# Optimization experiments

Measured on AMD Instinct MI355X. Metric: run time of the kernel, lower is better.

The kernel has to match this reference:

```python
import jax, jax.numpy as jnp
import numpy as np

L, B, T, H = 3, 128, 256, 512  # layers, batch, seq_max_len, n_hidden


def setup_inputs() -> dict:
    key = jax.random.key(0)
    k0, k1, k2 = jax.random.split(key, 3)
    scale = 1.0 / np.sqrt(H).astype(np.float32)
    x = jax.random.normal(k0, (B, T, H), jnp.float32)
    kernels = jax.random.normal(k1, (L, H, 3 * H), jnp.float32) * scale
    rec_kernels = jax.random.normal(k2, (L, H, 3 * H), jnp.float32) * scale
    biases = jnp.zeros((L, 2, 3 * H), jnp.float32)  # [input_bias, recurrent_bias] (reset_after=True)
    return {"x": x, "kernels": kernels, "rec_kernels": rec_kernels, "biases": biases}


def _gru_layer(x, h0, Wk, Wu, b):
    # x: [B,T,D], h0: [B,H], Wk: [D,3H], Wu: [H,3H], b: [2,3H]
    # Keras GRU, reset_after=True, gate order (z, r, h)
    xp = jnp.einsum('btd,dh->bth', x, Wk) + b[0]  # precompute input projections
    br = b[1]

    def step(h, xp_t):
        rec = h @ Wu + br                      # [B,3H]
        xz, xr, xh = jnp.split(xp_t, 3, axis=-1)
        rz, rr, rh = jnp.split(rec, 3, axis=-1)
        z = jax.nn.sigmoid(xz + rz)
        r = jax.nn.sigmoid(xr + rr)
        hh = jnp.tanh(xh + r * rh)
        h_new = z * h + (1.0 - z) * hh
        return h_new, h_new

    last_h, seq = jax.lax.scan(step, h0, jnp.swapaxes(xp, 0, 1))  # seq: [T,B,H]
    return jnp.swapaxes(seq, 0, 1), last_h


def reference(x, kernels, rec_kernels, biases):
    Bc, Tc, _ = x.shape
    Hd = kernels.shape[2] // 3
    state = None
    for l in range(kernels.shape[0]):
        # layer l>0 receives previous layer's final state as initial_state
        h0 = jnp.zeros((Bc, Hd), x.dtype) if state is None else state
        x, state = _gru_layer(x, h0, kernels[l], rec_kernels[l], biases[l])
    # tf.reshape(states, (-1, H)) then tf.split(seq_max_len, axis=0) -> stack == reshape to [T, B, H]
    states_h = x.reshape(-1, Hd).reshape(Tc, -1, Hd)
    return states_h, state
```

## Files before the change

### kernel.cpp

```cpp
#include <hip/hip_runtime.h>
#include <hip/hip_bf16.h>

#define NL  3
#define NB  128
#define NT  256
#define NH  512
#define NH3 1536
#define NBH (NB*NH)
#define NM  (NB*NT)

typedef __bf16 bf16x8 __attribute__((ext_vector_type(8)));
typedef float  floatx4 __attribute__((ext_vector_type(4)));
typedef __hip_bfloat16 bf16;
typedef unsigned long long u64;

__device__ __forceinline__ floatx4 mfma16(bf16x8 a, bf16x8 b, floatx4 c) {
  return __builtin_amdgcn_mfma_f32_16x16x32_bf16(a, b, c, 0, 0, 0);
}
__device__ __forceinline__ void gload16(const void* g, void* l) {
  __builtin_amdgcn_global_load_lds(
      (const __attribute__((address_space(1))) unsigned int*)g,
      (__attribute__((address_space(3))) unsigned int*)l, 16, 0, 0);
}
__device__ __forceinline__ float fsig(float x)  { return 1.0f / (1.0f + __expf(-x)); }
__device__ __forceinline__ float ftanh(float x) { return 2.0f / (1.0f + __expf(-2.0f*x)) - 1.0f; }
__device__ __forceinline__ float b2f(unsigned short u) {
  unsigned v = (unsigned)u << 16; float f; __builtin_memcpy(&f, &v, 4); return f;
}
__device__ __forceinline__ unsigned short f2b(float f) {
  bf16 h = __float2bfloat16(f); unsigned short u; __builtin_memcpy(&u, &h, 2); return u;
}
__device__ __forceinline__ u64 ald(const u64* p) {
  return __hip_atomic_load(p, __ATOMIC_RELAXED, __HIP_MEMORY_SCOPE_AGENT);
}
__device__ __forceinline__ void ast(u64* p, u64 v) {
  __hip_atomic_store(p, v, __ATOMIC_RELAXED, __HIP_MEMORY_SCOPE_AGENT);
}

__global__ void transpose_cvt_kernel(const float* __restrict__ in, bf16* __restrict__ out) {
  __shared__ float tile[32][33];
  int l = blockIdx.z;
  int n0 = blockIdx.x * 32, k0 = blockIdx.y * 32;
  const float* src = in + (size_t)l * NH * NH3;
  bf16* dst = out + (size_t)l * NH3 * NH;
  int tx = threadIdx.x, ty = threadIdx.y;
#pragma unroll
  for (int i = 0; i < 4; i++)
    tile[ty + 8*i][tx] = src[(size_t)(k0 + ty + 8*i) * NH3 + n0 + tx];
  __syncthreads();
#pragma unroll
  for (int i = 0; i < 4; i++)
    dst[(size_t)(n0 + ty + 8*i) * NH + k0 + tx] = __float2bfloat16(tile[tx][ty + 8*i]);
}

__global__ void cvt_x_kernel(const float* __restrict__ in, bf16* __restrict__ out) {
  size_t i = (size_t)blockIdx.x * blockDim.x + threadIdx.x;
  float4 v = ((const float4*)in)[i];
  ushort4 pk;
  pk.x = f2b(v.x); pk.y = f2b(v.y); pk.z = f2b(v.z); pk.w = f2b(v.w);
  ((ushort4*)out)[i] = pk;
}

__global__ void __launch_bounds__(256, 2) gemm_xp_kernel(
    const bf16* __restrict__ A, const bf16* __restrict__ Bt,
    const float* __restrict__ bias, bf16* __restrict__ C, int a_mode)
{
  __shared__ char alds[16384];
  __shared__ char blds[16384];
  int tid = threadIdx.x;
  int lane = tid & 63, w = tid >> 6;
  int mblk = blockIdx.x, nblk = blockIdx.y;
  int wm = w >> 1, wn = w & 1;
  int klane = (lane >> 4) * 8;
  int r0 = 2*w*16 + (lane & 15);
  size_t arow0, arow1;
  if (a_mode == 0) {
    arow0 = ((size_t)r0 * NT + mblk) * NH;
    arow1 = ((size_t)(r0 + 16) * NT + mblk) * NH;
  } else {
    arow0 = (size_t)(mblk*128 + r0) * NH;
    arow1 = arow0 + (size_t)16 * NH;
  }
  size_t brow0 = (size_t)(nblk*128 + 2*w*16 + (lane & 15)) * NH;
  size_t brow1 = brow0 + (size_t)16 * NH;

  floatx4 acc[4][4];
#pragma unroll
  for (int i = 0; i < 4; i++)
#pragma unroll
    for (int j = 0; j < 4; j++) acc[i][j] = (floatx4){0.f, 0.f, 0.f, 0.f};

  for (int kk = 0; kk < 8; kk++) {
    int kb = kk*64 + klane;
#pragma unroll
    for (int kt = 0; kt < 2; kt++) {
      int kg = kb + kt*32;
      gload16(A  + arow0 + kg, alds + (kt*8 + 2*w    ) * 1024);
      gload16(A  + arow1 + kg, alds + (kt*8 + 2*w + 1) * 1024);
      gload16(Bt + brow0 + kg, blds + (kt*8 + 2*w    ) * 1024);
      gload16(Bt + brow1 + kg, blds + (kt*8 + 2*w + 1) * 1024);
    }
    __syncthreads();
#pragma unroll
    for (int kt = 0; kt < 2; kt++) {
      bf16x8 af[4], bfr[4];
#pragma unroll
      for (int i = 0; i < 4; i++) af[i]  = *(const bf16x8*)(alds + ((kt*8 + wm*4 + i)*64 + lane)*16);
#pragma unroll
      for (int j = 0; j < 4; j++) bfr[j] = *(const bf16x8*)(blds + ((kt*8 + wn*4 + j)*64 + lane)*16);
#pragma unroll
      for (int i = 0; i < 4; i++)
#pragma unroll
        for (int j = 0; j < 4; j++)
          acc[i][j] = mfma16(af[i], bfr[j], acc[i][j]);
    }
    __syncthreads();
  }
  int cl = lane & 15, rbase = (lane >> 4) * 4;
#pragma unroll
  for (int i = 0; i < 4; i++) {
    int gm = mblk*128 + wm*64 + i*16 + rbase;
#pragma unroll
    for (int j = 0; j < 4; j++) {
      int gn = nblk*128 + wn*64 + j*16 + cl;
      float bv = bias[gn];
#pragma unroll
      for (int r = 0; r < 4; r++)
        C[(size_t)(gm + r) * NH3 + gn] = __float2bfloat16(acc[i][j][r] + bv);
    }
  }
}

__global__ void __launch_bounds__(512, 2) gru_scan_kernel(
    const bf16*  __restrict__ wuT,
    const float* __restrict__ br,
    const bf16*  __restrict__ xp,
    bf16*        __restrict__ seq,
    float*       __restrict__ hlast,
    float*       __restrict__ out,
    unsigned*    __restrict__ cnt,
    unsigned tgtbase, int layer)
{
  __shared__ __align__(16) char h_raw[16384];
  __shared__ int deadflag;
  int tid = threadIdx.x, lane = tid & 63, w = tid >> 6;
  int g = blockIdx.x >> 2, c = blockIdx.x & 3;
  int bb0 = g * 16;
  int r16 = lane & 15, h4 = lane >> 4;
  int srow = tid & 15, ssc = tid >> 4;
  if (tid == 0) deadflag = 0;

  bf16x8 wf[3][16];
  float  bv[3][4];
#pragma unroll
  for (int G = 0; G < 3; G++) {
    const bf16* wrow = wuT + ((size_t)(G*NH + c*128 + w*16 + r16)) * NH + h4*8;
#pragma unroll
    for (int kt = 0; kt < 16; kt++) wf[G][kt] = *(const bf16x8*)(wrow + kt*32);
#pragma unroll
    for (int q = 0; q < 4; q++) bv[G][q] = br[G*NH + c*128 + w*16 + h4*4 + q];
  }

  float hreg[4];
  if (layer == 0) {
    hreg[0] = hreg[1] = hreg[2] = hreg[3] = 0.0f;
  } else {
    const float* hsrc = hlast + (size_t)(bb0 + r16) * NH + c*128 + w*16 + h4*4;
    float4 v = *(const float4*)hsrc;
    hreg[0] = v.x; hreg[1] = v.y; hreg[2] = v.z; hreg[3] = v.w;
  }

  u64* seqU = (u64*)seq;

  for (int t = 0; t < NT; t++) {
    const u64* xq = (const u64*)(xp + ((size_t)t*NB + bb0 + r16)*NH3 + c*128 + w*16 + h4*4);
    u64 xv0 = xq[0], xv1 = xq[128], xv2 = xq[256];

    if (t > 0) {
      if (tid == 0) {
        unsigned tgt = tgtbase + 4u * (unsigned)t;
        long sp = 0;
        while (__hip_atomic_load(cnt + g, __ATOMIC_RELAXED, __HIP_MEMORY_SCOPE_AGENT) < tgt) {
          __builtin_amdgcn_s_sleep(1);
          if (++sp > (1L << 22)) { deadflag = 1; break; }
        }
      }
      __syncthreads();
      if (deadflag) return;
    }

    if (layer == 0 && t == 0) {
      *(int4*)(h_raw + tid*32)      = (int4){0,0,0,0};
      *(int4*)(h_raw + tid*32 + 16) = (int4){0,0,0,0};
    } else {
      int slot = (t == 0) ? NT : t;
      const u64* src = seqU + ((size_t)slot*NBH + (size_t)(bb0 + srow)*NH) / 4;
#pragma unroll
      for (int d = 0; d < 2; d++) {
        int sc = ssc + d*32;
        u64 q0 = ald(src + sc*2), q1 = ald(src + sc*2 + 1);
        u64* dst = (u64*)(h_raw + (((sc >> 2)*64) + (sc & 3)*16 + srow)*16);
        dst[0] = q0; dst[1] = q1;
      }
    }
    __syncthreads();

    floatx4 ac0 = (floatx4){0,0,0,0}, ac1 = (floatx4){0,0,0,0}, ac2 = (floatx4){0,0,0,0};
#pragma unroll
    for (int kt = 0; kt < 16; kt++) {
      bf16x8 hb = *(const bf16x8*)(h_raw + (kt*64 + lane)*16);
      ac0 = mfma16(wf[0][kt], hb, ac0);
      ac1 = mfma16(wf[1][kt], hb, ac1);
      ac2 = mfma16(wf[2][kt], hb, ac2);
    }

    unsigned short pk[4];
#pragma unroll
    for (int q = 0; q < 4; q++) {
      float rz = ac0[q] + bv[0][q];
      float rr = ac1[q] + bv[1][q];
      float rh = ac2[q] + bv[2][q];
      float xz = b2f((unsigned short)(xv0 >> (16*q)));
      float xr = b2f((unsigned short)(xv1 >> (16*q)));
      float xh = b2f((unsigned short)(xv2 >> (16*q)));
      float z  = fsig(xz + rz);
      float r  = fsig(xr + rr);
      float hh = ftanh(xh + r * rh);
      float hn = z * hreg[q] + (1.0f - z) * hh;
      hreg[q] = hn;
      pk[q] = f2b(hn);
    }
    u64 pv; __builtin_memcpy(&pv, pk, 8);
    ast(seqU + ((size_t)(t+1)*NBH + (size_t)(bb0 + r16)*NH)/4 + c*32 + w*4 + h4, pv);

    if (layer == 2) {
      float* o = out + ((size_t)(bb0 + r16)*NT + t)*NH + c*128 + w*16 + h4*4;
      *(float4*)o = (float4){hreg[0], hreg[1], hreg[2], hreg[3]};
      if (t == NT - 1) {
        float* o2 = out + (size_t)NM*NH + (size_t)(bb0 + r16)*NH + c*128 + w*16 + h4*4;
        *(float4*)o2 = (float4){hreg[0], hreg[1], hreg[2], hreg[3]};
      }
    } else if (t == NT - 1) {
      float* o = hlast + (size_t)(bb0 + r16)*NH + c*128 + w*16 + h4*4;
      *(float4*)o = (float4){hreg[0], hreg[1], hreg[2], hreg[3]};
    }

    __syncthreads();
    if (tid == 0 && t < NT - 1)
      __hip_atomic_fetch_add(cnt + g, 1u, __ATOMIC_RELAXED, __HIP_MEMORY_SCOPE_AGENT);
  }
}

extern "C" void kernel_launch(void* const* d_in, const int* in_sizes, int n_in,
                              void* d_out, int out_size, void* d_ws, size_t ws_size,
                              hipStream_t stream) {
  const float* x   = (const float*)d_in[0];
  const float* wk  = (const float*)d_in[1];
  const float* wu  = (const float*)d_in[2];
  const float* bis = (const float*)d_in[3];
  float* out = (float*)d_out;

  const size_t REQ = 144048192;
  if (ws_size < REQ) {
    hipMemsetAsync(d_out, 0, (size_t)out_size * 4, stream);
    return;
  }
  char* ws = (char*)d_ws;
  bf16*  wkT   = (bf16*)(ws);
  bf16*  wuT   = (bf16*)(ws + 4718592);
  bf16*  xp    = (bf16*)(ws + 9437184);
  bf16*  seq   = (bf16*)(ws + 110100480);
  bf16*  xb    = seq;
  float* hlast = (float*)(ws + 143785984);
  unsigned* cnt = (unsigned*)(ws + 144048128);

  hipMemsetAsync(cnt, 0, 64, stream);
  transpose_cvt_kernel<<<dim3(48,16,3), dim3(32,8), 0, stream>>>(wk, wkT);
  transpose_cvt_kernel<<<dim3(48,16,3), dim3(32,8), 0, stream>>>(wu, wuT);
  cvt_x_kernel<<<(NM*NH/4)/256, 256, 0, stream>>>(x, xb);

  const size_t WS = (size_t)NH3 * NH;

  gemm_xp_kernel<<<dim3(256,12), 256, 0, stream>>>(xb, wkT, bis + 0*2*NH3, xp, 0);
  gru_scan_kernel<<<32, 512, 0, stream>>>(wuT, bis + 0*2*NH3 + NH3, xp,
      seq, hlast, nullptr, cnt, 0u, 0);
  gemm_xp_kernel<<<dim3(256,12), 256, 0, stream>>>(seq + NBH, wkT + WS, bis + 1*2*NH3, xp, 1);
  gru_scan_kernel<<<32, 512, 0, stream>>>(wuT + WS, bis + 1*2*NH3 + NH3, xp,
      seq, hlast, nullptr, cnt, 1020u, 1);
  gemm_xp_kernel<<<dim3(256,12), 256, 0, stream>>>(seq + NBH, wkT + 2*WS, bis + 2*2*NH3, xp, 1);
  gru_scan_kernel<<<32, 512, 0, stream>>>(wuT + 2*WS, bis + 2*2*NH3 + NH3, xp,
      seq, hlast, out, cnt, 2040u, 2);

  (void)in_sizes; (void)n_in; (void)out_size; (void)ws_size;
}
```

Before: 3.490 ms.

## Replace counter barrier with tagged data flags and double-buffered hidden state exchange

Removes the per-step atomic counter barrier between the four blocks that share a batch group. Each block now publishes its new hidden slice into a double-buffered exchange buffer, with a step tag packed into the upper 32 bits of every 64-bit word. Consumers spin on the data itself until all tags match, which drops one __syncthreads and the atomic round trip per step. The cost is twice the store traffic into the exchange buffer, polling reads that every thread issues, and reliance on each 64-bit store being seen whole.

```diff
diff --git a/kernel.cpp b/kernel.cpp
--- a/kernel.cpp
+++ b/kernel.cpp
@@ -138,11 +138,11 @@
     bf16*        __restrict__ seq,
     float*       __restrict__ hlast,
     float*       __restrict__ out,
-    unsigned*    __restrict__ cnt,
-    unsigned tgtbase, int layer)
+    u64*         __restrict__ xbuf,
+    unsigned tagbase, int layer)
 {
-  __shared__ __align__(16) char h_raw[16384];
-  __shared__ int deadflag;
+  __shared__ __align__(16) char h_raw[2][16384];
+  __shared__ volatile int deadflag;
   int tid = threadIdx.x, lane = tid & 63, w = tid >> 6;
   int g = blockIdx.x >> 2, c = blockIdx.x & 3;
   int bb0 = g * 16;
@@ -171,44 +171,63 @@
   }
 
   u64* seqU = (u64*)seq;
+  const size_t PARU = (size_t)128 * 256;
+  u64* pubp = xbuf + ((size_t)(bb0 + r16) * 256 + (size_t)(c*64 + w*8 + h4*2));
 
   for (int t = 0; t < NT; t++) {
+    if (t == 0) {
+      if (layer == 0) {
+        *(int4*)(h_raw[0] + tid*32)      = (int4){0,0,0,0};
+        *(int4*)(h_raw[0] + tid*32 + 16) = (int4){0,0,0,0};
+      } else {
+        const u64* src = seqU + ((size_t)NT*NBH + (size_t)(bb0 + srow)*NH) / 4;
+#pragma unroll
+        for (int d = 0; d < 2; d++) {
+          int sc = ssc + d*32;
+          u64 q0 = ald(src + sc*2), q1 = ald(src + sc*2 + 1);
+          u64* dst = (u64*)(h_raw[0] + (((sc >> 2)*64) + (sc & 3)*16 + srow)*16);
+          dst[0] = q0; dst[1] = q1;
+        }
+      }
+    } else {
+      const u64* sb = xbuf + (size_t)(t & 1)*PARU + (size_t)(bb0 + srow)*256;
+      unsigned want = tagbase + (unsigned)t;
+      int j0 = ssc, j1 = ssc + 32, j2 = ssc + 64, j3 = ssc + 96;
+      u64 a0=0, a1=0, b0=0, b1=0, c0=0, c1=0, d0=0, d1=0;
+      int it = 0;
+      while (!deadflag) {
+        a0 = ald(sb + 2*j0); a1 = ald(sb + 2*j0 + 1);
+        b0 = ald(sb + 2*j1); b1 = ald(sb + 2*j1 + 1);
+        c0 = ald(sb + 2*j2); c1 = ald(sb + 2*j2 + 1);
+        d0 = ald(sb + 2*j3); d1 = ald(sb + 2*j3 + 1);
+        bool ok = ((unsigned)(a0 >> 32) == want) & ((unsigned)(a1 >> 32) == want) &
+                  ((unsigned)(b0 >> 32) == want) & ((unsigned)(b1 >> 32) == want) &
+                  ((unsigned)(c0 >> 32) == want) & ((unsigned)(c1 >> 32) == want) &
+                  ((unsigned)(d0 >> 32) == want) & ((unsigned)(d1 >> 32) == want);
+        if (ok) break;
+        if (++it > (1 << 17)) { deadflag = 1; break; }
+      }
+      char* hb = h_raw[t & 1];
+      *(u64*)(hb + (((j0>>3)*64 + ((j0>>1)&3)*16 + srow)*16 + (j0&1)*8)) =
+          (u64)(unsigned)a0 | ((u64)(unsigned)a1 << 32);
+      *(u64*)(hb + (((j1>>3)*64 + ((j1>>1)&3)*16 + srow)*16 + (j1&1)*8)) =
+          (u64)(unsigned)b0 | ((u64)(unsigned)b1 << 32);
+      *(u64*)(hb + (((j2>>3)*64 + ((j2>>1)&3)*16 + srow)*16 + (j2&1)*8)) =
+          (u64)(unsigned)c0 | ((u64)(unsigned)c1 << 32);
+      *(u64*)(hb + (((j3>>3)*64 + ((j3>>1)&3)*16 + srow)*16 + (j3&1)*8)) =
+          (u64)(unsigned)d0 | ((u64)(unsigned)d1 << 32);
+    }
+
     const u64* xq = (const u64*)(xp + ((size_t)t*NB + bb0 + r16)*NH3 + c*128 + w*16 + h4*4);
     u64 xv0 = xq[0], xv1 = xq[128], xv2 = xq[256];
 
-    if (t > 0) {
-      if (tid == 0) {
-        unsigned tgt = tgtbase + 4u * (unsigned)t;
-        long sp = 0;
-        while (__hip_atomic_load(cnt + g, __ATOMIC_RELAXED, __HIP_MEMORY_SCOPE_AGENT) < tgt) {
-          __builtin_amdgcn_s_sleep(1);
-          if (++sp > (1L << 22)) { deadflag = 1; break; }
-        }
-      }
-      __syncthreads();
-      if (deadflag) return;
-    }
-
-    if (layer == 0 && t == 0) {
-      *(int4*)(h_raw + tid*32)      = (int4){0,0,0,0};
-      *(int4*)(h_raw + tid*32 + 16) = (int4){0,0,0,0};
-    } else {
-      int slot = (t == 0) ? NT : t;
-      const u64* src = seqU + ((size_t)slot*NBH + (size_t)(bb0 + srow)*NH) / 4;
-#pragma unroll
-      for (int d = 0; d < 2; d++) {
-        int sc = ssc + d*32;
-        u64 q0 = ald(src + sc*2), q1 = ald(src + sc*2 + 1);
-        u64* dst = (u64*)(h_raw + (((sc >> 2)*64) + (sc & 3)*16 + srow)*16);
-        dst[0] = q0; dst[1] = q1;
-      }
-    }
     __syncthreads();
 
+    const char* hbR = h_raw[t & 1];
     floatx4 ac0 = (floatx4){0,0,0,0}, ac1 = (floatx4){0,0,0,0}, ac2 = (floatx4){0,0,0,0};
 #pragma unroll
     for (int kt = 0; kt < 16; kt++) {
-      bf16x8 hb = *(const bf16x8*)(h_raw + (kt*64 + lane)*16);
+      bf16x8 hb = *(const bf16x8*)(hbR + (kt*64 + lane)*16);
       ac0 = mfma16(wf[0][kt], hb, ac0);
       ac1 = mfma16(wf[1][kt], hb, ac1);
       ac2 = mfma16(wf[2][kt], hb, ac2);
@@ -231,7 +250,15 @@
       pk[q] = f2b(hn);
     }
     u64 pv; __builtin_memcpy(&pv, pk, 8);
-    ast(seqU + ((size_t)(t+1)*NBH + (size_t)(bb0 + r16)*NH)/4 + c*32 + w*4 + h4, pv);
+
+    if (t < NT - 1) {
+      u64 tg = (u64)(tagbase + (unsigned)t + 1u) << 32;
+      u64* pp = pubp + (size_t)((t + 1) & 1) * PARU;
+      ast(pp,     ((u64)(unsigned)(pv & 0xffffffffu)) | tg);
+      ast(pp + 1, ((u64)(unsigned)(pv >> 32))         | tg);
+    }
+    if (layer != 2)
+      seqU[((size_t)(t+1)*NBH + (size_t)(bb0 + r16)*NH)/4 + c*32 + w*4 + h4] = pv;
 
     if (layer == 2) {
       float* o = out + ((size_t)(bb0 + r16)*NT + t)*NH + c*128 + w*16 + h4*4;
@@ -244,10 +271,6 @@
       float* o = hlast + (size_t)(bb0 + r16)*NH + c*128 + w*16 + h4*4;
       *(float4*)o = (float4){hreg[0], hreg[1], hreg[2], hreg[3]};
     }
-
-    __syncthreads();
-    if (tid == 0 && t < NT - 1)
-      __hip_atomic_fetch_add(cnt + g, 1u, __ATOMIC_RELAXED, __HIP_MEMORY_SCOPE_AGENT);
   }
 }
 
@@ -260,7 +283,7 @@
   const float* bis = (const float*)d_in[3];
   float* out = (float*)d_out;
 
-  const size_t REQ = 144048192;
+  const size_t REQ = 144572416;
   if (ws_size < REQ) {
     hipMemsetAsync(d_out, 0, (size_t)out_size * 4, stream);
     return;
@@ -272,9 +295,9 @@
   bf16*  seq   = (bf16*)(ws + 110100480);
   bf16*  xb    = seq;
   float* hlast = (float*)(ws + 143785984);
-  unsigned* cnt = (unsigned*)(ws + 144048128);
-
-  hipMemsetAsync(cnt, 0, 64, stream);
+  u64*   xbuf  = (u64*)(ws + 144048128);
+
+  hipMemsetAsync(xbuf, 0, 524288, stream);
   transpose_cvt_kernel<<<dim3(48,16,3), dim3(32,8), 0, stream>>>(wk, wkT);
   transpose_cvt_kernel<<<dim3(48,16,3), dim3(32,8), 0, stream>>>(wu, wuT);
   cvt_x_kernel<<<(NM*NH/4)/256, 256, 0, stream>>>(x, xb);
@@ -283,13 +306,13 @@
 
   gemm_xp_kernel<<<dim3(256,12), 256, 0, stream>>>(xb, wkT, bis + 0*2*NH3, xp, 0);
   gru_scan_kernel<<<32, 512, 0, stream>>>(wuT, bis + 0*2*NH3 + NH3, xp,
-      seq, hlast, nullptr, cnt, 0u, 0);
+      seq, hlast, nullptr, xbuf, 0u, 0);
   gemm_xp_kernel<<<dim3(256,12), 256, 0, stream>>>(seq + NBH, wkT + WS, bis + 1*2*NH3, xp, 1);
   gru_scan_kernel<<<32, 512, 0, stream>>>(wuT + WS, bis + 1*2*NH3 + NH3, xp,
-      seq, hlast, nullptr, cnt, 1020u, 1);
+      seq, hlast, nullptr, xbuf, 256u, 1);
   gemm_xp_kernel<<<dim3(256,12), 256, 0, stream>>>(seq + NBH, wkT + 2*WS, bis + 2*2*NH3, xp, 1);
   gru_scan_kernel<<<32, 512, 0, stream>>>(wuT + 2*WS, bis + 2*2*NH3 + NH3, xp,
-      seq, hlast, out, cnt, 2040u, 2);
+      seq, hlast, out, xbuf, 512u, 2);
 
   (void)in_sizes; (void)n_in; (void)out_size; (void)ws_size;
 }
```

Result: slower. 4.762 ms (+36.4%).
